# Kernel optimization log

Measured on AMD Instinct MI355X. Metric: run time of the kernel, lower is better.

Reference implementation:

```python
import jax, jax.numpy as jnp
import numpy as np

N_WIRES = 12
DIM = 2 ** N_WIRES  # 4096 = seq_len * embed_dim

_H = np.array([[1, 1], [1, -1]], dtype=np.complex64) / np.sqrt(2.0)
_CNOT = np.array([[1, 0, 0, 0],
                  [0, 1, 0, 0],
                  [0, 0, 0, 1],
                  [0, 0, 1, 0]], dtype=np.complex64)
_SWAP = np.array([[1, 0, 0, 0],
                  [0, 0, 1, 0],
                  [0, 1, 0, 0],
                  [0, 0, 0, 1]], dtype=np.complex64)

def _cp_mat(theta):
    m = np.eye(4, dtype=np.complex64)
    m[3, 3] = np.exp(1j * theta)
    return m

def _apply_gate(state, U, wires):
    # state: (B,) + (2,)*N_WIRES ; U: (2^k, 2^k) acting on `wires` (wire 0 = MSB = axis 1)
    k = len(wires)
    src = [w + 1 for w in wires]
    dst = list(range(1, k + 1))
    st = jnp.moveaxis(state, src, dst)
    sh = st.shape
    st = st.reshape(sh[0], 2 ** k, -1)
    st = jnp.einsum('ij,bjr->bir', jnp.asarray(U), st)
    return jnp.moveaxis(st.reshape(sh), dst, src)

def _cnot_ring(state):
    for i in range(N_WIRES):
        state = _apply_gate(state, _CNOT, [i, (i + 1) % N_WIRES])
    return state

def _qft(state):
    for m in range(N_WIRES - 1, 0, -1):
        state = _apply_gate(state, _H, [m])
        for i in range(m):
            state = _apply_gate(state, _cp_mat(np.pi / 2 ** (m - i)), [i, m])
    for i in range(N_WIRES // 2):
        state = _apply_gate(state, _SWAP, [i, N_WIRES - i - 1])
    return state

def _full_unitary(state, U):
    # dense 2^n x 2^n unitary over the whole register: psi' = U @ psi
    b = state.shape[0]
    flat = state.reshape(b, DIM)
    return jnp.einsum('ij,bj->bi', U, flat).reshape(state.shape)

def setup_inputs() -> dict:
    key = jax.random.key(0)
    k1, k2, k3 = jax.random.split(key, 3)
    x = jax.random.normal(k1, (128, 64, 64), dtype=jnp.float32)
    scale = DIM ** -0.5  # keep applied matrices roughly norm-preserving
    U_re = jax.random.normal(k2, (4, DIM, DIM), dtype=jnp.float32) * scale
    U_im = jax.random.normal(k3, (4, DIM, DIM), dtype=jnp.float32) * scale
    return {"x": x, "U_re": U_re, "U_im": U_im}

def reference(x, U_re, U_im):
    B, S, E = x.shape
    flat = x.reshape(B, S * E)
    pad = DIM - flat.shape[1]
    if pad > 0:
        flat = jnp.pad(flat, ((0, 0), (0, pad)))
    # StateEncoder: L2-normalize and lift to complex statevector
    norm = jnp.sqrt(jnp.sum(flat * flat, axis=-1, keepdims=True))
    psi = (flat / norm).astype(jnp.complex64)
    state = psi.reshape((B,) + (2,) * N_WIRES)
    U = (U_re + 1j * U_im).astype(jnp.complex64)
    # vqc(0)
    state = _full_unitary(state, U[0])
    state = _cnot_ring(state)
    state = _full_unitary(state, U[1])
    # qft
    state = _qft(state)
    # vqc(1)
    state = _full_unitary(state, U[2])
    state = _cnot_ring(state)
    state = _full_unitary(state, U[3])
    out = jnp.abs(state.reshape(B, DIM))
    return out.reshape(B, S, E)
```

## Files before the change

### kernel.cpp

```cpp
#include <hip/hip_runtime.h>
#include <hip/hip_bf16.h>
#include <math.h>

#define N_WIRES 12
#define DIM     4096
#define BATCH   128
#define BD      (BATCH*DIM)
#define BM      128
#define BN      32
#define BK      64
#define KS      4
#define KCHUNK  (DIM / KS)

typedef __attribute__((ext_vector_type(4))) float f32x4;
typedef __attribute__((ext_vector_type(4))) unsigned int u32x4;
typedef __bf16 bf16x8 __attribute__((ext_vector_type(8)));
typedef __attribute__((ext_vector_type(8))) unsigned short us8;
typedef __attribute__((ext_vector_type(4))) unsigned short us4;

__device__ __forceinline__ f32x4 mfma16(bf16x8 a, bf16x8 b, f32x4 c){
  return __builtin_amdgcn_mfma_f32_16x16x32_bf16(a, b, c, 0, 0, 0);
}

__device__ __forceinline__ void gload16(const void* g, void* l){
  __builtin_amdgcn_global_load_lds(
    (const __attribute__((address_space(1))) unsigned int*)g,
    (__attribute__((address_space(3))) unsigned int*)l, 16, 0, 0);
}

__device__ __forceinline__ float bf2f(unsigned short u){
  union { unsigned int i; float f; } cv; cv.i = ((unsigned int)u) << 16; return cv.f;
}

__device__ __forceinline__ int swz(int j, int b){
  return (j & ~63) | (((((j >> 3) & 7) ^ (b & 7))) << 3) | (j & 7);
}

__global__ void k_normalize(const float* __restrict__ x, __hip_bfloat16* __restrict__ dst){
  const int b = blockIdx.x, t = threadIdx.x;
  const float4* xr = reinterpret_cast<const float4*>(x + (size_t)b * DIM);
  float4 v[4];
  float ss = 0.f;
  #pragma unroll
  for (int r = 0; r < 4; ++r){
    v[r] = xr[t*4 + r];
    ss += v[r].x*v[r].x + v[r].y*v[r].y + v[r].z*v[r].z + v[r].w*v[r].w;
  }
  #pragma unroll
  for (int off = 32; off > 0; off >>= 1) ss += __shfl_down(ss, off);
  __shared__ float sred[4];
  if ((t & 63) == 0) sred[t >> 6] = ss;
  __syncthreads();
  const float inv = 1.f / sqrtf(sred[0] + sred[1] + sred[2] + sred[3]);
  #pragma unroll
  for (int h = 0; h < 2; ++h){
    union { __bf16 e[8]; us8 s; } pk;
    const float* vv = reinterpret_cast<const float*>(&v[h*2]);
    #pragma unroll
    for (int j = 0; j < 8; ++j) pk.e[j] = (__bf16)(vv[j] * inv);
    const int j0 = t*16 + h*8;
    *reinterpret_cast<us8*>(dst + (size_t)b*DIM + swz(j0, b)) = pk.s;
  }
}

template<bool CIN>
__global__ __launch_bounds__(256, 2) void k_gemm(
    const float* __restrict__ Ure, const float* __restrict__ Uim,
    const __hip_bfloat16* __restrict__ X, __hip_bfloat16* __restrict__ P)
{
  constexpr int NCC = CIN ? 2 : 1;
  constexpr int NT  = KCHUNK / BK;
  __shared__ __bf16 Xs[2][NCC*BM*BK];
  __shared__ __bf16 Us[2][2*BN*BK];
  const int t = threadIdx.x;
  const int lane = t & 63, wid = t >> 6;
  const int n0 = blockIdx.x * BN;
  const int kb = blockIdx.y * KCHUNK;

  const f32x4 z4 = {0.f,0.f,0.f,0.f};
  f32x4 acc[2][2][2];
  #pragma unroll
  for (int mi = 0; mi < 2; ++mi)
    #pragma unroll
    for (int ni = 0; ni < 2; ++ni){ acc[mi][ni][0] = z4; acc[mi][ni][1] = z4; }

  auto stageX = [&](int kk, int bf){
    #pragma unroll
    for (int r = 0; r < NCC*4; ++r){
      const int idx = r*256 + t;
      const int c = idx >> 10, ci = idx & 1023;
      const int row = ci >> 3, sc = ci & 7;
      gload16(X + (size_t)c*BD + (size_t)row*DIM + kb + kk + sc*8, &Xs[bf][idx*8]);
    }
  };
  auto loadU = [&](int kk, float4 (&uv)[4]){
    #pragma unroll
    for (int r = 0; r < 4; ++r){
      const int idx = r*256 + t;
      const int c = idx >> 9, ci = idx & 511;
      const int row = ci >> 4, q = ci & 15;
      const float* us = c ? Uim : Ure;
      uv[r] = *reinterpret_cast<const float4*>(us + (size_t)(n0 + row)*DIM + kb + kk + q*4);
    }
  };
  auto writeU = [&](const float4 (&uv)[4], int bf){
    #pragma unroll
    for (int r = 0; r < 4; ++r){
      const int idx = r*256 + t;
      const int c = idx >> 9, ci = idx & 511;
      const int row = ci >> 4, q = ci & 15;
      union { __bf16 h[4]; unsigned long long u; } pk;
      pk.h[0]=(__bf16)uv[r].x; pk.h[1]=(__bf16)uv[r].y;
      pk.h[2]=(__bf16)uv[r].z; pk.h[3]=(__bf16)uv[r].w;
      const int e = (((q >> 1) ^ (row & 7)) << 3) | ((q & 1) << 2);
      *reinterpret_cast<unsigned long long*>(&Us[bf][c*BN*BK + row*BK + e]) = pk.u;
    }
  };
  auto compute = [&](int bf){
    #pragma unroll
    for (int ks = 0; ks < 2; ++ks){
      const int lc = ks*4 + (lane >> 4);
      bf16x8 ar[2], ai[2], br[2], bi[2];
      #pragma unroll
      for (int mi = 0; mi < 2; ++mi){
        const int row = wid*32 + mi*16 + (lane & 15);
        const int off = row*BK + ((lc ^ (row & 7)) << 3);
        ar[mi] = *reinterpret_cast<const bf16x8*>(&Xs[bf][off]);
        if (CIN) ai[mi] = *reinterpret_cast<const bf16x8*>(&Xs[bf][BM*BK + off]);
      }
      #pragma unroll
      for (int ni = 0; ni < 2; ++ni){
        const int row = ni*16 + (lane & 15);
        const int off = row*BK + ((lc ^ (row & 7)) << 3);
        br[ni] = *reinterpret_cast<const bf16x8*>(&Us[bf][off]);
        bi[ni] = *reinterpret_cast<const bf16x8*>(&Us[bf][BN*BK + off]);
      }
      #pragma unroll
      for (int mi = 0; mi < 2; ++mi){
        bf16x8 an = ar[mi];
        if (CIN){
          const u32x4 negu = __builtin_bit_cast(u32x4, ai[mi]) ^ 0x80008000u;
          an = __builtin_bit_cast(bf16x8, negu);
        }
        #pragma unroll
        for (int ni = 0; ni < 2; ++ni){
          acc[mi][ni][0] = mfma16(br[ni], ar[mi], acc[mi][ni][0]);
          acc[mi][ni][1] = mfma16(bi[ni], ar[mi], acc[mi][ni][1]);
          if (CIN){
            acc[mi][ni][0] = mfma16(bi[ni], an,     acc[mi][ni][0]);
            acc[mi][ni][1] = mfma16(br[ni], ai[mi], acc[mi][ni][1]);
          }
        }
      }
    }
  };

  float4 uvA[4], uvB[4], uvC[4];
  loadU(0, uvA);
  loadU(BK, uvB);
  stageX(0, 0);

#define GSTEP(TT, UC, UN, WAITS)                                               \
  {                                                                            \
    if ((TT) + 1 < NT) stageX(((TT)+1)*BK, ((TT)+1) & 1);                      \
    if ((TT) + 2 < NT) loadU(((TT)+2)*BK, UN);                                 \
    asm volatile("s_waitcnt vmcnt(" WAITS ")" ::: "memory");                   \
    __builtin_amdgcn_sched_barrier(0);                                         \
    writeU(UC, (TT) & 1);                                                      \
    asm volatile("s_waitcnt lgkmcnt(0)" ::: "memory");                         \
    __builtin_amdgcn_s_barrier();                                              \
    compute((TT) & 1);                                                         \
    __builtin_amdgcn_sched_barrier(0);                                         \
    __builtin_amdgcn_s_barrier();                                              \
  }

  GSTEP(0,  uvA, uvC, "12")
  GSTEP(1,  uvB, uvA, "16")
  GSTEP(2,  uvC, uvB, "16")
  GSTEP(3,  uvA, uvC, "16")
  GSTEP(4,  uvB, uvA, "16")
  GSTEP(5,  uvC, uvB, "16")
  GSTEP(6,  uvA, uvC, "16")
  GSTEP(7,  uvB, uvA, "16")
  GSTEP(8,  uvC, uvB, "16")
  GSTEP(9,  uvA, uvC, "16")
  GSTEP(10, uvB, uvA, "16")
  GSTEP(11, uvC, uvB, "16")
  GSTEP(12, uvA, uvC, "16")
  GSTEP(13, uvB, uvA, "16")
  GSTEP(14, uvC, uvB, "12")
  GSTEP(15, uvA, uvB, "0")
#undef GSTEP

  __hip_bfloat16* pre = P + (size_t)(blockIdx.y*2 + 0)*BD;
  __hip_bfloat16* pim = P + (size_t)(blockIdx.y*2 + 1)*BD;
  #pragma unroll
  for (int mi = 0; mi < 2; ++mi)
    #pragma unroll
    for (int ni = 0; ni < 2; ++ni){
      const int b  = wid*32 + mi*16 + (lane & 15);
      const int nb = n0 + ni*16 + (lane >> 4)*4;
      union { __hip_bfloat16 h[4]; us4 v; } pk0, pk1;
      #pragma unroll
      for (int j = 0; j < 4; ++j){
        pk0.h[j] = __float2bfloat16(acc[mi][ni][0][j]);
        pk1.h[j] = __float2bfloat16(acc[mi][ni][1][j]);
      }
      *reinterpret_cast<us4*>(pre + (size_t)b*DIM + nb) = pk0.v;
      *reinterpret_cast<us4*>(pim + (size_t)b*DIM + nb) = pk1.v;
    }
}

__device__ __forceinline__ int cnot_dst(int x){
  #pragma unroll
  for (int i = 0; i < 12; ++i){
    const int cb = 11 - i;
    const int tb = 11 - ((i + 1) % 12);
    x ^= ((x >> cb) & 1) << tb;
  }
  return x;
}
__device__ __forceinline__ int cnot_inv(int x){
  #pragma unroll
  for (int i = 11; i >= 0; --i){
    const int cb = 11 - i;
    const int tb = 11 - ((i + 1) % 12);
    x ^= ((x >> cb) & 1) << tb;
  }
  return x;
}

__global__ void k_perm(const __hip_bfloat16* __restrict__ P, __hip_bfloat16* __restrict__ dst){
  __shared__ float sre[DIM];
  __shared__ float sim[DIM];
  const int b = blockIdx.x, t = threadIdx.x;
  #pragma unroll
  for (int h = 0; h < 2; ++h){
    const int m0 = (t*2 + h) * 8;
    float re[8], im[8];
    #pragma unroll
    for (int j = 0; j < 8; ++j){ re[j] = 0.f; im[j] = 0.f; }
    #pragma unroll
    for (int s = 0; s < KS; ++s){
      const us8 vr = *reinterpret_cast<const us8*>(P + (size_t)(s*2+0)*BD + (size_t)b*DIM + m0);
      const us8 vi = *reinterpret_cast<const us8*>(P + (size_t)(s*2+1)*BD + (size_t)b*DIM + m0);
      #pragma unroll
      for (int j = 0; j < 8; ++j){ re[j] += bf2f(vr[j]); im[j] += bf2f(vi[j]); }
    }
    #pragma unroll
    for (int j = 0; j < 8; ++j){ sre[m0+j] = re[j]; sim[m0+j] = im[j]; }
  }
  __syncthreads();
  #pragma unroll
  for (int h = 0; h < 2; ++h){
    const int E0 = (t*2 + h) * 8;
    const int k0 = swz(E0, b);
    union { __hip_bfloat16 e[8]; us8 s; } pr, pi;
    #pragma unroll
    for (int j = 0; j < 8; ++j){
      const int m = cnot_inv(k0 + j);
      pr.e[j] = __float2bfloat16(sre[m]);
      pi.e[j] = __float2bfloat16(sim[m]);
    }
    *reinterpret_cast<us8*>(dst + (size_t)b*DIM + E0) = pr.s;
    *reinterpret_cast<us8*>(dst + (size_t)BD + (size_t)b*DIM + E0) = pi.s;
  }
}

__global__ void k_abs(const __hip_bfloat16* __restrict__ P, float* __restrict__ dst){
  const int g = blockIdx.x * 256 + threadIdx.x;
  const int b = g >> 9;
  const int m0 = (g & 511) * 8;
  float re[8], im[8];
  #pragma unroll
  for (int j = 0; j < 8; ++j){ re[j] = 0.f; im[j] = 0.f; }
  #pragma unroll
  for (int s = 0; s < KS; ++s){
    const us8 vr = *reinterpret_cast<const us8*>(P + (size_t)(s*2+0)*BD + (size_t)b*DIM + m0);
    const us8 vi = *reinterpret_cast<const us8*>(P + (size_t)(s*2+1)*BD + (size_t)b*DIM + m0);
    #pragma unroll
    for (int j = 0; j < 8; ++j){ re[j] += bf2f(vr[j]); im[j] += bf2f(vi[j]); }
  }
  #pragma unroll
  for (int j = 0; j < 8; ++j)
    dst[(size_t)b*DIM + m0 + j] = sqrtf(re[j]*re[j] + im[j]*im[j]);
}

__global__ void k_qft(const __hip_bfloat16* __restrict__ P, __hip_bfloat16* __restrict__ out){
  __shared__ float sre[DIM];
  __shared__ float sim[DIM];
  const int b = blockIdx.x, t = threadIdx.x;
  {
    const int c  = t >> 9;
    const int m0 = (t & 511) * 8;
    float v[8];
    #pragma unroll
    for (int j = 0; j < 8; ++j) v[j] = 0.f;
    #pragma unroll
    for (int s = 0; s < KS; ++s){
      const us8 vv = *reinterpret_cast<const us8*>(P + (size_t)(s*2+c)*BD + (size_t)b*DIM + m0);
      #pragma unroll
      for (int j = 0; j < 8; ++j) v[j] += bf2f(vv[j]);
    }
    float* s0 = c ? sim : sre;
    #pragma unroll
    for (int j = 0; j < 8; ++j) s0[m0+j] = v[j];
  }
  __syncthreads();
  const float rs2 = 0.70710678118654752440f;
  const float pscale = 3.14159265358979323846f * 0x1p-32f;
  for (int m = 11; m >= 1; --m){
    const int p = 11 - m;
    const int mask = 1 << p;
    #pragma unroll
    for (int q = t; q < 2048; q += 1024){
      const int i0 = ((q & ~(mask-1)) << 1) | (q & (mask-1));
      const int i1 = i0 | mask;
      const float r0 = sre[i0], s0 = sim[i0], r1 = sre[i1], s1 = sim[i1];
      sre[i0] = (r0 + r1) * rs2; sim[i0] = (s0 + s1) * rs2;
      sre[i1] = (r0 - r1) * rs2; sim[i1] = (s0 - s1) * rs2;
    }
    __syncthreads();
    #pragma unroll
    for (int q = t; q < 2048; q += 1024){
      const int i1 = (((q & ~(mask-1)) << 1) | (q & (mask-1))) | mask;
      const unsigned u = (unsigned)(i1 >> (p + 1));
      const float phi = (float)__brev(u) * pscale;
      float cc, ss;
      __sincosf(phi, &ss, &cc);
      const float r = sre[i1], q2 = sim[i1];
      sre[i1] = r*cc - q2*ss;
      sim[i1] = r*ss + q2*cc;
    }
    __syncthreads();
  }
  {
    const int c  = t >> 9;
    const int E0 = (t & 511) * 8;
    const int i0 = swz(E0, b);
    const float* s0 = c ? sim : sre;
    union { __hip_bfloat16 e[8]; us8 s; } pk;
    #pragma unroll
    for (int j = 0; j < 8; ++j){
      const int rsrc = (int)(__brev((unsigned)(i0 + j)) >> 20);
      pk.e[j] = __float2bfloat16(s0[rsrc]);
    }
    *reinterpret_cast<us8*>(out + (size_t)c*BD + (size_t)b*DIM + E0) = pk.s;
  }
}

extern "C" void kernel_launch(void* const* d_in, const int* in_sizes, int n_in,
                              void* d_out, int out_size, void* d_ws, size_t ws_size,
                              hipStream_t stream){
  const float* x   = (const float*)d_in[0];
  const float* Ure = (const float*)d_in[1];
  const float* Uim = (const float*)d_in[2];
  float* out = (float*)d_out;

  __hip_bfloat16* P  = (__hip_bfloat16*)d_ws;
  __hip_bfloat16* B0 = P + (size_t)KS*2*BD;
  __hip_bfloat16* B1 = B0 + (size_t)2*BD;
  const size_t UST = (size_t)DIM*DIM;
  const dim3 gg(DIM/BN, KS);

  k_normalize<<<BATCH, 256, 0, stream>>>(x, B0);
  k_gemm<false><<<gg, 256, 0, stream>>>(Ure, Uim, B0, P);
  k_perm<<<BATCH, 256, 0, stream>>>(P, B1);
  k_gemm<true><<<gg, 256, 0, stream>>>(Ure + UST, Uim + UST, B1, P);
  k_qft<<<BATCH, 1024, 0, stream>>>(P, B0);
  k_gemm<true><<<gg, 256, 0, stream>>>(Ure + 2*UST, Uim + 2*UST, B0, P);
  k_perm<<<BATCH, 256, 0, stream>>>(P, B1);
  k_gemm<true><<<gg, 256, 0, stream>>>(Ure + 3*UST, Uim + 3*UST, B1, P);
  k_abs<<<BD/2048, 256, 0, stream>>>(P, out);
}
```

Measured before the change: 192.2 us.

## Load X fragments directly from global, double split-K, widen permutation kernel

The GEMM drops LDS staging of the state matrix X and has each lane read its MFMA fragments straight from global memory, which also removes the swizzled layouts in the normalize, QFT and permute kernels. Split-K goes from 4 to 8 chunks and launch bounds rise to 4 blocks per CU. Together these aim to raise occupancy and cut LDS traffic and barriers. The permute kernel is split across two blocks per batch row with 512 threads each. The trade-off is uncoalesced, uncached-in-LDS global reads of X, twice the partial-sum traffic in P, and more reduction work in every consumer kernel.

```diff
diff --git a/kernel.cpp b/kernel.cpp
--- a/kernel.cpp
+++ b/kernel.cpp
@@ -9,7 +9,7 @@
 #define BM      128
 #define BN      32
 #define BK      64
-#define KS      4
+#define KS      8
 #define KCHUNK  (DIM / KS)
 
 typedef __attribute__((ext_vector_type(4))) float f32x4;
@@ -22,19 +22,10 @@
   return __builtin_amdgcn_mfma_f32_16x16x32_bf16(a, b, c, 0, 0, 0);
 }
 
-__device__ __forceinline__ void gload16(const void* g, void* l){
-  __builtin_amdgcn_global_load_lds(
-    (const __attribute__((address_space(1))) unsigned int*)g,
-    (__attribute__((address_space(3))) unsigned int*)l, 16, 0, 0);
-}
-
 __device__ __forceinline__ float bf2f(unsigned short u){
   union { unsigned int i; float f; } cv; cv.i = ((unsigned int)u) << 16; return cv.f;
 }
 
-__device__ __forceinline__ int swz(int j, int b){
-  return (j & ~63) | (((((j >> 3) & 7) ^ (b & 7))) << 3) | (j & 7);
-}
 
 __global__ void k_normalize(const float* __restrict__ x, __hip_bfloat16* __restrict__ dst){
   const int b = blockIdx.x, t = threadIdx.x;
@@ -58,19 +49,16 @@
     const float* vv = reinterpret_cast<const float*>(&v[h*2]);
     #pragma unroll
     for (int j = 0; j < 8; ++j) pk.e[j] = (__bf16)(vv[j] * inv);
-    const int j0 = t*16 + h*8;
-    *reinterpret_cast<us8*>(dst + (size_t)b*DIM + swz(j0, b)) = pk.s;
+    *reinterpret_cast<us8*>(dst + (size_t)b*DIM + t*16 + h*8) = pk.s;
   }
 }
 
 template<bool CIN>
-__global__ __launch_bounds__(256, 2) void k_gemm(
+__global__ __launch_bounds__(256, 4) void k_gemm(
     const float* __restrict__ Ure, const float* __restrict__ Uim,
     const __hip_bfloat16* __restrict__ X, __hip_bfloat16* __restrict__ P)
 {
-  constexpr int NCC = CIN ? 2 : 1;
-  constexpr int NT  = KCHUNK / BK;
-  __shared__ __bf16 Xs[2][NCC*BM*BK];
+  constexpr int NT = KCHUNK / BK;
   __shared__ __bf16 Us[2][2*BN*BK];
   const int t = threadIdx.x;
   const int lane = t & 63, wid = t >> 6;
@@ -84,15 +72,8 @@
     #pragma unroll
     for (int ni = 0; ni < 2; ++ni){ acc[mi][ni][0] = z4; acc[mi][ni][1] = z4; }
 
-  auto stageX = [&](int kk, int bf){
-    #pragma unroll
-    for (int r = 0; r < NCC*4; ++r){
-      const int idx = r*256 + t;
-      const int c = idx >> 10, ci = idx & 1023;
-      const int row = ci >> 3, sc = ci & 7;
-      gload16(X + (size_t)c*BD + (size_t)row*DIM + kb + kk + sc*8, &Xs[bf][idx*8]);
-    }
-  };
+  const __hip_bfloat16* Xb = X + (size_t)(wid*32 + (lane & 15))*DIM + kb + ((lane >> 4) << 3);
+
   auto loadU = [&](int kk, float4 (&uv)[4]){
     #pragma unroll
     for (int r = 0; r < 4; ++r){
@@ -116,81 +97,72 @@
       *reinterpret_cast<unsigned long long*>(&Us[bf][c*BN*BK + row*BK + e]) = pk.u;
     }
   };
-  auto compute = [&](int bf){
-    #pragma unroll
-    for (int ks = 0; ks < 2; ++ks){
-      const int lc = ks*4 + (lane >> 4);
-      bf16x8 ar[2], ai[2], br[2], bi[2];
-      #pragma unroll
-      for (int mi = 0; mi < 2; ++mi){
-        const int row = wid*32 + mi*16 + (lane & 15);
-        const int off = row*BK + ((lc ^ (row & 7)) << 3);
-        ar[mi] = *reinterpret_cast<const bf16x8*>(&Xs[bf][off]);
-        if (CIN) ai[mi] = *reinterpret_cast<const bf16x8*>(&Xs[bf][BM*BK + off]);
-      }
-      #pragma unroll
-      for (int ni = 0; ni < 2; ++ni){
-        const int row = ni*16 + (lane & 15);
-        const int off = row*BK + ((lc ^ (row & 7)) << 3);
-        br[ni] = *reinterpret_cast<const bf16x8*>(&Us[bf][off]);
-        bi[ni] = *reinterpret_cast<const bf16x8*>(&Us[bf][BN*BK + off]);
-      }
-      #pragma unroll
-      for (int mi = 0; mi < 2; ++mi){
-        bf16x8 an = ar[mi];
-        if (CIN){
-          const u32x4 negu = __builtin_bit_cast(u32x4, ai[mi]) ^ 0x80008000u;
-          an = __builtin_bit_cast(bf16x8, negu);
-        }
-        #pragma unroll
-        for (int ni = 0; ni < 2; ++ni){
-          acc[mi][ni][0] = mfma16(br[ni], ar[mi], acc[mi][ni][0]);
-          acc[mi][ni][1] = mfma16(bi[ni], ar[mi], acc[mi][ni][1]);
-          if (CIN){
-            acc[mi][ni][0] = mfma16(bi[ni], an,     acc[mi][ni][0]);
-            acc[mi][ni][1] = mfma16(br[ni], ai[mi], acc[mi][ni][1]);
-          }
-        }
-      }
-    }
-  };
-
-  float4 uvA[4], uvB[4], uvC[4];
+
+#define COMPUTE(TT, BF)                                                        \
+  {                                                                            \
+    _Pragma("unroll")                                                          \
+    for (int ks = 0; ks < 2; ++ks){                                            \
+      const int lc = ks*4 + (lane >> 4);                                       \
+      bf16x8 ar[2], ai[2], br[2], bi[2];                                       \
+      _Pragma("unroll")                                                        \
+      for (int mi = 0; mi < 2; ++mi){                                          \
+        const __hip_bfloat16* xp = Xb + (size_t)mi*16*DIM + (TT)*BK + ks*32;   \
+        ar[mi] = *reinterpret_cast<const bf16x8*>(xp);                         \
+        if (CIN) ai[mi] = *reinterpret_cast<const bf16x8*>(xp + BD);           \
+      }                                                                        \
+      _Pragma("unroll")                                                        \
+      for (int ni = 0; ni < 2; ++ni){                                          \
+        const int row = ni*16 + (lane & 15);                                   \
+        const int off = row*BK + ((lc ^ (row & 7)) << 3);                      \
+        br[ni] = *reinterpret_cast<const bf16x8*>(&Us[BF][off]);               \
+        bi[ni] = *reinterpret_cast<const bf16x8*>(&Us[BF][BN*BK + off]);       \
+      }                                                                        \
+      _Pragma("unroll")                                                        \
+      for (int mi = 0; mi < 2; ++mi){                                          \
+        bf16x8 an = ar[mi];                                                    \
+        if (CIN){                                                              \
+          const u32x4 negu = __builtin_bit_cast(u32x4, ai[mi]) ^ 0x80008000u;  \
+          an = __builtin_bit_cast(bf16x8, negu);                               \
+        }                                                                      \
+        _Pragma("unroll")                                                      \
+        for (int ni = 0; ni < 2; ++ni){                                        \
+          acc[mi][ni][0] = mfma16(br[ni], ar[mi], acc[mi][ni][0]);             \
+          acc[mi][ni][1] = mfma16(bi[ni], ar[mi], acc[mi][ni][1]);             \
+          if (CIN){                                                            \
+            acc[mi][ni][0] = mfma16(bi[ni], an,     acc[mi][ni][0]);           \
+            acc[mi][ni][1] = mfma16(br[ni], ai[mi], acc[mi][ni][1]);           \
+          }                                                                    \
+        }                                                                      \
+      }                                                                        \
+    }                                                                          \
+  }
+
+  float4 uvA[4], uvB[4];
   loadU(0, uvA);
-  loadU(BK, uvB);
-  stageX(0, 0);
 
 #define GSTEP(TT, UC, UN, WAITS)                                               \
   {                                                                            \
-    if ((TT) + 1 < NT) stageX(((TT)+1)*BK, ((TT)+1) & 1);                      \
-    if ((TT) + 2 < NT) loadU(((TT)+2)*BK, UN);                                 \
+    if ((TT) + 1 < NT) loadU(((TT)+1)*BK, UN);                                 \
     asm volatile("s_waitcnt vmcnt(" WAITS ")" ::: "memory");                   \
     __builtin_amdgcn_sched_barrier(0);                                         \
     writeU(UC, (TT) & 1);                                                      \
     asm volatile("s_waitcnt lgkmcnt(0)" ::: "memory");                         \
     __builtin_amdgcn_s_barrier();                                              \
-    compute((TT) & 1);                                                         \
+    COMPUTE(TT, (TT) & 1);                                                     \
     __builtin_amdgcn_sched_barrier(0);                                         \
     __builtin_amdgcn_s_barrier();                                              \
   }
 
-  GSTEP(0,  uvA, uvC, "12")
-  GSTEP(1,  uvB, uvA, "16")
-  GSTEP(2,  uvC, uvB, "16")
-  GSTEP(3,  uvA, uvC, "16")
-  GSTEP(4,  uvB, uvA, "16")
-  GSTEP(5,  uvC, uvB, "16")
-  GSTEP(6,  uvA, uvC, "16")
-  GSTEP(7,  uvB, uvA, "16")
-  GSTEP(8,  uvC, uvB, "16")
-  GSTEP(9,  uvA, uvC, "16")
-  GSTEP(10, uvB, uvA, "16")
-  GSTEP(11, uvC, uvB, "16")
-  GSTEP(12, uvA, uvC, "16")
-  GSTEP(13, uvB, uvA, "16")
-  GSTEP(14, uvC, uvB, "12")
-  GSTEP(15, uvA, uvB, "0")
+  GSTEP(0, uvA, uvB, "4")
+  GSTEP(1, uvB, uvA, "4")
+  GSTEP(2, uvA, uvB, "4")
+  GSTEP(3, uvB, uvA, "4")
+  GSTEP(4, uvA, uvB, "4")
+  GSTEP(5, uvB, uvA, "4")
+  GSTEP(6, uvA, uvB, "4")
+  GSTEP(7, uvB, uvA, "0")
 #undef GSTEP
+#undef COMPUTE
 
   __hip_bfloat16* pre = P + (size_t)(blockIdx.y*2 + 0)*BD;
   __hip_bfloat16* pim = P + (size_t)(blockIdx.y*2 + 1)*BD;
@@ -211,15 +183,6 @@
     }
 }
 
-__device__ __forceinline__ int cnot_dst(int x){
-  #pragma unroll
-  for (int i = 0; i < 12; ++i){
-    const int cb = 11 - i;
-    const int tb = 11 - ((i + 1) % 12);
-    x ^= ((x >> cb) & 1) << tb;
-  }
-  return x;
-}
 __device__ __forceinline__ int cnot_inv(int x){
   #pragma unroll
   for (int i = 11; i >= 0; --i){
@@ -231,39 +194,34 @@
 }
 
 __global__ void k_perm(const __hip_bfloat16* __restrict__ P, __hip_bfloat16* __restrict__ dst){
-  __shared__ float sre[DIM];
-  __shared__ float sim[DIM];
-  const int b = blockIdx.x, t = threadIdx.x;
+  __shared__ float s[2][DIM];
+  const int b = blockIdx.x >> 1, half = blockIdx.x & 1;
+  const int t = threadIdx.x;
   #pragma unroll
   for (int h = 0; h < 2; ++h){
-    const int m0 = (t*2 + h) * 8;
-    float re[8], im[8];
-    #pragma unroll
-    for (int j = 0; j < 8; ++j){ re[j] = 0.f; im[j] = 0.f; }
-    #pragma unroll
-    for (int s = 0; s < KS; ++s){
-      const us8 vr = *reinterpret_cast<const us8*>(P + (size_t)(s*2+0)*BD + (size_t)b*DIM + m0);
-      const us8 vi = *reinterpret_cast<const us8*>(P + (size_t)(s*2+1)*BD + (size_t)b*DIM + m0);
+    const int idx = h*512 + t;
+    const int c = idx >> 9, m0 = (idx & 511) * 8;
+    float v[8];
+    #pragma unroll
+    for (int j = 0; j < 8; ++j) v[j] = 0.f;
+    #pragma unroll
+    for (int sp = 0; sp < KS; ++sp){
+      const us8 vv = *reinterpret_cast<const us8*>(P + (size_t)(sp*2+c)*BD + (size_t)b*DIM + m0);
       #pragma unroll
-      for (int j = 0; j < 8; ++j){ re[j] += bf2f(vr[j]); im[j] += bf2f(vi[j]); }
-    }
-    #pragma unroll
-    for (int j = 0; j < 8; ++j){ sre[m0+j] = re[j]; sim[m0+j] = im[j]; }
+      for (int j = 0; j < 8; ++j) v[j] += bf2f(vv[j]);
+    }
+    #pragma unroll
+    for (int j = 0; j < 8; ++j) s[c][m0+j] = v[j];
   }
   __syncthreads();
-  #pragma unroll
-  for (int h = 0; h < 2; ++h){
-    const int E0 = (t*2 + h) * 8;
-    const int k0 = swz(E0, b);
-    union { __hip_bfloat16 e[8]; us8 s; } pr, pi;
-    #pragma unroll
-    for (int j = 0; j < 8; ++j){
-      const int m = cnot_inv(k0 + j);
-      pr.e[j] = __float2bfloat16(sre[m]);
-      pi.e[j] = __float2bfloat16(sim[m]);
-    }
-    *reinterpret_cast<us8*>(dst + (size_t)b*DIM + E0) = pr.s;
-    *reinterpret_cast<us8*>(dst + (size_t)BD + (size_t)b*DIM + E0) = pi.s;
+  {
+    const int c  = t >> 8;
+    const int k0 = half*2048 + (t & 255) * 8;
+    union { __hip_bfloat16 e[8]; us8 v; } pk;
+    #pragma unroll
+    for (int j = 0; j < 8; ++j)
+      pk.e[j] = __float2bfloat16(s[c][cnot_inv(k0 + j)]);
+    *reinterpret_cast<us8*>(dst + (size_t)c*BD + (size_t)b*DIM + k0) = pk.v;
   }
 }
 
@@ -275,9 +233,9 @@
   #pragma unroll
   for (int j = 0; j < 8; ++j){ re[j] = 0.f; im[j] = 0.f; }
   #pragma unroll
-  for (int s = 0; s < KS; ++s){
-    const us8 vr = *reinterpret_cast<const us8*>(P + (size_t)(s*2+0)*BD + (size_t)b*DIM + m0);
-    const us8 vi = *reinterpret_cast<const us8*>(P + (size_t)(s*2+1)*BD + (size_t)b*DIM + m0);
+  for (int sp = 0; sp < KS; ++sp){
+    const us8 vr = *reinterpret_cast<const us8*>(P + (size_t)(sp*2+0)*BD + (size_t)b*DIM + m0);
+    const us8 vi = *reinterpret_cast<const us8*>(P + (size_t)(sp*2+1)*BD + (size_t)b*DIM + m0);
     #pragma unroll
     for (int j = 0; j < 8; ++j){ re[j] += bf2f(vr[j]); im[j] += bf2f(vi[j]); }
   }
@@ -297,8 +255,8 @@
     #pragma unroll
     for (int j = 0; j < 8; ++j) v[j] = 0.f;
     #pragma unroll
-    for (int s = 0; s < KS; ++s){
-      const us8 vv = *reinterpret_cast<const us8*>(P + (size_t)(s*2+c)*BD + (size_t)b*DIM + m0);
+    for (int sp = 0; sp < KS; ++sp){
+      const us8 vv = *reinterpret_cast<const us8*>(P + (size_t)(sp*2+c)*BD + (size_t)b*DIM + m0);
       #pragma unroll
       for (int j = 0; j < 8; ++j) v[j] += bf2f(vv[j]);
     }
@@ -336,8 +294,7 @@
   }
   {
     const int c  = t >> 9;
-    const int E0 = (t & 511) * 8;
-    const int i0 = swz(E0, b);
+    const int i0 = (t & 511) * 8;
     const float* s0 = c ? sim : sre;
     union { __hip_bfloat16 e[8]; us8 s; } pk;
     #pragma unroll
@@ -345,7 +302,7 @@
       const int rsrc = (int)(__brev((unsigned)(i0 + j)) >> 20);
       pk.e[j] = __float2bfloat16(s0[rsrc]);
     }
-    *reinterpret_cast<us8*>(out + (size_t)c*BD + (size_t)b*DIM + E0) = pk.s;
+    *reinterpret_cast<us8*>(out + (size_t)c*BD + (size_t)b*DIM + i0) = pk.s;
   }
 }
 
@@ -365,11 +322,11 @@
 
   k_normalize<<<BATCH, 256, 0, stream>>>(x, B0);
   k_gemm<false><<<gg, 256, 0, stream>>>(Ure, Uim, B0, P);
-  k_perm<<<BATCH, 256, 0, stream>>>(P, B1);
+  k_perm<<<2*BATCH, 512, 0, stream>>>(P, B1);
   k_gemm<true><<<gg, 256, 0, stream>>>(Ure + UST, Uim + UST, B1, P);
   k_qft<<<BATCH, 1024, 0, stream>>>(P, B0);
   k_gemm<true><<<gg, 256, 0, stream>>>(Ure + 2*UST, Uim + 2*UST, B0, P);
-  k_perm<<<BATCH, 256, 0, stream>>>(P, B1);
+  k_perm<<<2*BATCH, 512, 0, stream>>>(P, B1);
   k_gemm<true><<<gg, 256, 0, stream>>>(Ure + 3*UST, Uim + 3*UST, B1, P);
   k_abs<<<BD/2048, 256, 0, stream>>>(P, out);
 }
```

Result: slower. 233.4 us (+21.4%).

## Deepen GEMM U-prefetch pipeline to four stages and split perm kernel across blocks

Applied to the files above, without the earlier changes.

The GEMM kernel now keeps five register buffers for U tiles and issues global loads four K-steps ahead instead of two, with the vmcnt wait counts adjusted to match. This is meant to hide more of the global-memory latency when streaming the large U matrices. The permutation kernel now runs two blocks of 512 threads per batch row, each writing half of the output, to raise parallelism in that memory-bound step. In exchange, the GEMM uses more VGPRs, which can lower occupancy, and each perm block redundantly reduces the full row.

```diff
diff --git a/kernel.cpp b/kernel.cpp
--- a/kernel.cpp
+++ b/kernel.cpp
@@ -155,15 +155,17 @@
     }
   };
 
-  float4 uvA[4], uvB[4], uvC[4];
+  float4 uvA[4], uvB[4], uvC[4], uvD[4], uvE[4];
   loadU(0, uvA);
-  loadU(BK, uvB);
   stageX(0, 0);
+  loadU(1*BK, uvB);
+  loadU(2*BK, uvC);
+  loadU(3*BK, uvD);
 
 #define GSTEP(TT, UC, UN, WAITS)                                               \
   {                                                                            \
     if ((TT) + 1 < NT) stageX(((TT)+1)*BK, ((TT)+1) & 1);                      \
-    if ((TT) + 2 < NT) loadU(((TT)+2)*BK, UN);                                 \
+    if ((TT) + 4 < NT) loadU(((TT)+4)*BK, UN);                                 \
     asm volatile("s_waitcnt vmcnt(" WAITS ")" ::: "memory");                   \
     __builtin_amdgcn_sched_barrier(0);                                         \
     writeU(UC, (TT) & 1);                                                      \
@@ -174,21 +176,21 @@
     __builtin_amdgcn_s_barrier();                                              \
   }
 
-  GSTEP(0,  uvA, uvC, "12")
+  GSTEP(0,  uvA, uvE, "12")
   GSTEP(1,  uvB, uvA, "16")
   GSTEP(2,  uvC, uvB, "16")
-  GSTEP(3,  uvA, uvC, "16")
-  GSTEP(4,  uvB, uvA, "16")
-  GSTEP(5,  uvC, uvB, "16")
-  GSTEP(6,  uvA, uvC, "16")
-  GSTEP(7,  uvB, uvA, "16")
-  GSTEP(8,  uvC, uvB, "16")
-  GSTEP(9,  uvA, uvC, "16")
-  GSTEP(10, uvB, uvA, "16")
-  GSTEP(11, uvC, uvB, "16")
-  GSTEP(12, uvA, uvC, "16")
-  GSTEP(13, uvB, uvA, "16")
-  GSTEP(14, uvC, uvB, "12")
+  GSTEP(3,  uvD, uvC, "16")
+  GSTEP(4,  uvE, uvD, "16")
+  GSTEP(5,  uvA, uvE, "16")
+  GSTEP(6,  uvB, uvA, "16")
+  GSTEP(7,  uvC, uvB, "16")
+  GSTEP(8,  uvD, uvC, "16")
+  GSTEP(9,  uvE, uvD, "16")
+  GSTEP(10, uvA, uvE, "16")
+  GSTEP(11, uvB, uvA, "16")
+  GSTEP(12, uvC, uvB, "12")
+  GSTEP(13, uvD, uvC, "8")
+  GSTEP(14, uvE, uvD, "8")
   GSTEP(15, uvA, uvB, "0")
 #undef GSTEP
 
@@ -211,15 +213,6 @@
     }
 }
 
-__device__ __forceinline__ int cnot_dst(int x){
-  #pragma unroll
-  for (int i = 0; i < 12; ++i){
-    const int cb = 11 - i;
-    const int tb = 11 - ((i + 1) % 12);
-    x ^= ((x >> cb) & 1) << tb;
-  }
-  return x;
-}
 __device__ __forceinline__ int cnot_inv(int x){
   #pragma unroll
   for (int i = 11; i >= 0; --i){
@@ -231,39 +224,35 @@
 }
 
 __global__ void k_perm(const __hip_bfloat16* __restrict__ P, __hip_bfloat16* __restrict__ dst){
-  __shared__ float sre[DIM];
-  __shared__ float sim[DIM];
-  const int b = blockIdx.x, t = threadIdx.x;
+  __shared__ float s[2][DIM];
+  const int b = blockIdx.x >> 1, half = blockIdx.x & 1;
+  const int t = threadIdx.x;
   #pragma unroll
   for (int h = 0; h < 2; ++h){
-    const int m0 = (t*2 + h) * 8;
-    float re[8], im[8];
-    #pragma unroll
-    for (int j = 0; j < 8; ++j){ re[j] = 0.f; im[j] = 0.f; }
-    #pragma unroll
-    for (int s = 0; s < KS; ++s){
-      const us8 vr = *reinterpret_cast<const us8*>(P + (size_t)(s*2+0)*BD + (size_t)b*DIM + m0);
-      const us8 vi = *reinterpret_cast<const us8*>(P + (size_t)(s*2+1)*BD + (size_t)b*DIM + m0);
-      #pragma unroll
-      for (int j = 0; j < 8; ++j){ re[j] += bf2f(vr[j]); im[j] += bf2f(vi[j]); }
-    }
-    #pragma unroll
-    for (int j = 0; j < 8; ++j){ sre[m0+j] = re[j]; sim[m0+j] = im[j]; }
+    const int idx = h*512 + t;
+    const int c = idx >> 9, m0 = (idx & 511) * 8;
+    float v[8];
+    #pragma unroll
+    for (int j = 0; j < 8; ++j) v[j] = 0.f;
+    #pragma unroll
+    for (int sp = 0; sp < KS; ++sp){
+      const us8 vv = *reinterpret_cast<const us8*>(P + (size_t)(sp*2+c)*BD + (size_t)b*DIM + m0);
+      #pragma unroll
+      for (int j = 0; j < 8; ++j) v[j] += bf2f(vv[j]);
+    }
+    #pragma unroll
+    for (int j = 0; j < 8; ++j) s[c][m0+j] = v[j];
   }
   __syncthreads();
-  #pragma unroll
-  for (int h = 0; h < 2; ++h){
-    const int E0 = (t*2 + h) * 8;
+  {
+    const int c  = t >> 8;
+    const int E0 = half*2048 + (t & 255) * 8;
     const int k0 = swz(E0, b);
-    union { __hip_bfloat16 e[8]; us8 s; } pr, pi;
-    #pragma unroll
-    for (int j = 0; j < 8; ++j){
-      const int m = cnot_inv(k0 + j);
-      pr.e[j] = __float2bfloat16(sre[m]);
-      pi.e[j] = __float2bfloat16(sim[m]);
-    }
-    *reinterpret_cast<us8*>(dst + (size_t)b*DIM + E0) = pr.s;
-    *reinterpret_cast<us8*>(dst + (size_t)BD + (size_t)b*DIM + E0) = pi.s;
+    union { __hip_bfloat16 e[8]; us8 v; } pk;
+    #pragma unroll
+    for (int j = 0; j < 8; ++j)
+      pk.e[j] = __float2bfloat16(s[c][cnot_inv(k0 + j)]);
+    *reinterpret_cast<us8*>(dst + (size_t)c*BD + (size_t)b*DIM + E0) = pk.v;
   }
 }
 
@@ -275,9 +264,9 @@
   #pragma unroll
   for (int j = 0; j < 8; ++j){ re[j] = 0.f; im[j] = 0.f; }
   #pragma unroll
-  for (int s = 0; s < KS; ++s){
-    const us8 vr = *reinterpret_cast<const us8*>(P + (size_t)(s*2+0)*BD + (size_t)b*DIM + m0);
-    const us8 vi = *reinterpret_cast<const us8*>(P + (size_t)(s*2+1)*BD + (size_t)b*DIM + m0);
+  for (int sp = 0; sp < KS; ++sp){
+    const us8 vr = *reinterpret_cast<const us8*>(P + (size_t)(sp*2+0)*BD + (size_t)b*DIM + m0);
+    const us8 vi = *reinterpret_cast<const us8*>(P + (size_t)(sp*2+1)*BD + (size_t)b*DIM + m0);
     #pragma unroll
     for (int j = 0; j < 8; ++j){ re[j] += bf2f(vr[j]); im[j] += bf2f(vi[j]); }
   }
@@ -297,8 +286,8 @@
     #pragma unroll
     for (int j = 0; j < 8; ++j) v[j] = 0.f;
     #pragma unroll
-    for (int s = 0; s < KS; ++s){
-      const us8 vv = *reinterpret_cast<const us8*>(P + (size_t)(s*2+c)*BD + (size_t)b*DIM + m0);
+    for (int sp = 0; sp < KS; ++sp){
+      const us8 vv = *reinterpret_cast<const us8*>(P + (size_t)(sp*2+c)*BD + (size_t)b*DIM + m0);
       #pragma unroll
       for (int j = 0; j < 8; ++j) v[j] += bf2f(vv[j]);
     }
@@ -365,11 +354,11 @@
 
   k_normalize<<<BATCH, 256, 0, stream>>>(x, B0);
   k_gemm<false><<<gg, 256, 0, stream>>>(Ure, Uim, B0, P);
-  k_perm<<<BATCH, 256, 0, stream>>>(P, B1);
+  k_perm<<<2*BATCH, 512, 0, stream>>>(P, B1);
   k_gemm<true><<<gg, 256, 0, stream>>>(Ure + UST, Uim + UST, B1, P);
   k_qft<<<BATCH, 1024, 0, stream>>>(P, B0);
   k_gemm<true><<<gg, 256, 0, stream>>>(Ure + 2*UST, Uim + 2*UST, B0, P);
-  k_perm<<<BATCH, 256, 0, stream>>>(P, B1);
+  k_perm<<<2*BATCH, 512, 0, stream>>>(P, B1);
   k_gemm<true><<<gg, 256, 0, stream>>>(Ure + 3*UST, Uim + 3*UST, B1, P);
   k_abs<<<BD/2048, 256, 0, stream>>>(P, out);
 }
```

Result: faster. 185.7 us, median of 2 (-3.4%).
